# Kernel optimization log

Measured on AMD Instinct MI355X. Metric: run time of the kernel, lower is better.

## Reference

```python
import jax, jax.numpy as jnp
import numpy as np

DIM = 1024
NUM_HEADS = 16
HEAD_DIM = DIM // NUM_HEADS  # 64
H = 32
W = 32
NREG = 8
B = 8
N = H * W + NREG  # 1032


def setup_inputs() -> dict:
    key = jax.random.key(0)
    ks = jax.random.split(key, 6)
    def rn(k, shape, std):
        return jax.random.normal(k, shape, dtype=jnp.float32) * std
    return {
        "x": rn(ks[0], (B, N, DIM), 1.0),
        "qkv_w": rn(ks[1], (3 * DIM, DIM), 0.02),
        "qkv_b": jnp.zeros((3 * DIM,), jnp.float32),
        "proj_w": rn(ks[2], (DIM, DIM), 0.02),
        "proj_b": jnp.zeros((DIM,), jnp.float32),
        "rel_pos_h": rn(ks[3], (2 * H - 1, HEAD_DIM), 0.02),
        "rel_pos_w": rn(ks[4], (2 * W - 1, HEAD_DIM), 0.02),
        "nreg": NREG,
        "cait": 0,
    }


def _rel_pos_table(rel_pos, size):
    # q_size == k_size == size -> relative index = i - j + (size - 1)
    coords = jnp.arange(size)[:, None] - jnp.arange(size)[None, :] + (size - 1)
    return rel_pos[coords]  # (size, size, head_dim)


def reference(x, qkv_w, qkv_b, proj_w, proj_b, rel_pos_h, rel_pos_w, nreg, cait):
    Bx, Nx, C = x.shape
    hd = C // NUM_HEADS
    scale = hd ** (-0.5)
    # qkv: (B, N, 3, nH, hd) -> (3, nH, B, N, hd) -> (3, nH*B, N, hd)
    qkv = (x @ qkv_w.T + qkv_b).reshape(Bx, Nx, 3, NUM_HEADS, hd)
    qkv = jnp.transpose(qkv, (2, 3, 0, 1, 4)).reshape(3, NUM_HEADS * Bx, Nx, hd)
    q, k, v = qkv[0], qkv[1], qkv[2]
    if cait:
        q = q[:, -nreg:]
    attn = jnp.einsum('bqd,bkd->bqk', q * scale, k)  # (nH*B, Nq, N)
    if not cait:
        hw = H * W
        Rh = _rel_pos_table(rel_pos_h, H)  # (H, H, hd)
        Rw = _rel_pos_table(rel_pos_w, W)  # (W, W, hd)
        r_q = q[:, :hw].reshape(-1, H, W, hd)  # unscaled q, grid tokens only
        rel_h = jnp.einsum('bhwc,hkc->bhwk', r_q, Rh)
        rel_w = jnp.einsum('bhwc,wkc->bhwk', r_q, Rw)
        grid = (attn[:, :hw, :hw].reshape(-1, H, W, H, W)
                + rel_h[:, :, :, :, None] + rel_w[:, :, :, None, :])
        attn = attn.at[:, :hw, :hw].set(grid.reshape(-1, hw, hw))
    attn = jax.nn.softmax(attn, axis=-1)
    out = jnp.einsum('bqk,bkd->bqd', attn, v)  # (nH*B, Nq, hd)
    out = out.reshape(NUM_HEADS, Bx, -1, hd)
    out = jnp.transpose(out, (1, 2, 0, 3)).reshape(Bx, -1, C)
    return out @ proj_w.T + proj_b
```

## Files before the change

kernel.cpp:

```cpp
#include <hip/hip_runtime.h>

#define BATCH 8
#define NTOK 1032
#define NPAD 1152
#define MTOT (BATCH*NTOK)
#define MPAD 8320

#define SCALE_Q 0.18033688011112042f
#define C2      5.770780163555854f

typedef __bf16 bf16x8 __attribute__((ext_vector_type(8)));
typedef float f32x4 __attribute__((ext_vector_type(4)));
typedef unsigned short us8 __attribute__((ext_vector_type(8)));
typedef unsigned short us4 __attribute__((ext_vector_type(4)));
typedef short s4 __attribute__((ext_vector_type(4)));

__device__ __forceinline__ unsigned short f2bf(float f){
  unsigned int u = __builtin_bit_cast(unsigned int, f);
  u += 0x7fffu + ((u >> 16) & 1u);
  return (unsigned short)(u >> 16);
}
__device__ __forceinline__ float bf2f(unsigned short u){
  return __builtin_bit_cast(float, (unsigned int)u << 16);
}

#define MFMA16(a,b,c) __builtin_amdgcn_mfma_f32_16x16x32_bf16( \
    __builtin_bit_cast(bf16x8,(a)), __builtin_bit_cast(bf16x8,(b)), (c), 0, 0, 0)
#define MFMAH(a,b,c) __builtin_amdgcn_mfma_f32_16x16x16bf16_1k( \
    __builtin_bit_cast(s4,(a)), __builtin_bit_cast(s4,(b)), (c), 0, 0, 0)

__device__ __forceinline__ void gl_lds16(const unsigned short* g, unsigned short* l){
  __builtin_amdgcn_global_load_lds(
      (const __attribute__((address_space(1))) unsigned int*)g,
      (__attribute__((address_space(3))) unsigned int*)l, 16, 0, 0);
}

__global__ __launch_bounds__(256) void cvt_f32_bf16(const float* __restrict__ in,
                                                    unsigned short* __restrict__ out, int n4){
  int i = blockIdx.x * 256 + threadIdx.x;
  if (i < n4){
    float4 v = reinterpret_cast<const float4*>(in)[i];
    us4 o; o.x = f2bf(v.x); o.y = f2bf(v.y); o.z = f2bf(v.z); o.w = f2bf(v.w);
    reinterpret_cast<us4*>(out)[i] = o;
  }
}

__global__ __launch_bounds__(256) void pad_zero(unsigned short* __restrict__ qb,
                                                unsigned short* __restrict__ kb,
                                                unsigned short* __restrict__ xb,
                                                unsigned short* __restrict__ ao){
  int i = blockIdx.x * 256 + threadIdx.x;
  const int t1 = 128 * (NPAD - NTOK) * 64;
  const int t2 = t1 + (MPAD - MTOT) * 1024;
  const int t3 = t2 + (MPAD - MTOT) * 1024;
  if (i < t1){
    int bh = i / ((NPAD - NTOK) * 64);
    int r  = (i / 64) % (NPAD - NTOK);
    int d  = i % 64;
    int idx = (bh * NPAD + NTOK + r) * 64 + d;
    qb[idx] = 0;
    kb[idx] = 0;
  } else if (i < t2){
    xb[(size_t)MTOT * 1024 + (i - t1)] = 0;
  } else if (i < t3){
    ao[(size_t)MTOT * 1024 + (i - t2)] = 0;
  }
}

__global__ __launch_bounds__(256,4) void qkv_gemm(
    const unsigned short* __restrict__ A,
    const unsigned short* __restrict__ Bw,
    const float* __restrict__ bias,
    unsigned short* __restrict__ qb,
    unsigned short* __restrict__ kb,
    unsigned short* __restrict__ vb)
{
  const int K = 1024;
  __shared__ __align__(16) unsigned short As[2][128*32];
  __shared__ __align__(16) unsigned short Bs[2][128*32];
  int tid = threadIdx.x;
  int id = blockIdx.x;
  int work = (id & 7) * 195 + (id >> 3);
  int m0 = (work / 24) * 128, n0 = (work % 24) * 128;
  int w = tid >> 6, lane = tid & 63, lr = lane & 15, lg = lane >> 4;
  int wr = w >> 1, wc = w & 1;
  int srow = lane >> 2;
  int scol = ((lane & 3) ^ ((lane >> 3) & 3)) * 8;
  int sa = (lg ^ ((lr >> 1) & 3)) * 8;
  f32x4 acc[4][4] = {};

  #pragma unroll
  for (int i = 0; i < 2; i++){
    int q = w * 2 + i;
    gl_lds16(&A [(size_t)(m0 + q*16 + srow) * K + scol], &As[0][q*512]);
    gl_lds16(&Bw[(size_t)(n0 + q*16 + srow) * K + scol], &Bs[0][q*512]);
  }

  for (int kt = 0; kt < 32; kt++){
    int cur = kt & 1;
    if (kt < 31){
      int k0 = (kt + 1) * 32;
      #pragma unroll
      for (int i = 0; i < 2; i++){
        int q = w * 2 + i;
        gl_lds16(&A [(size_t)(m0 + q*16 + srow) * K + k0 + scol], &As[cur^1][q*512]);
        gl_lds16(&Bw[(size_t)(n0 + q*16 + srow) * K + k0 + scol], &Bs[cur^1][q*512]);
      }
      asm volatile("s_waitcnt vmcnt(4)" ::: "memory");
    } else {
      asm volatile("s_waitcnt vmcnt(0)" ::: "memory");
    }
    __builtin_amdgcn_sched_barrier(0);
    __builtin_amdgcn_s_barrier();

    us8 a[4], b[4];
    #pragma unroll
    for (int mi = 0; mi < 4; mi++) a[mi] = *reinterpret_cast<const us8*>(&As[cur][(wr*64 + mi*16 + lr)*32 + sa]);
    #pragma unroll
    for (int ni = 0; ni < 4; ni++) b[ni] = *reinterpret_cast<const us8*>(&Bs[cur][(wc*64 + ni*16 + lr)*32 + sa]);
    #pragma unroll
    for (int mi = 0; mi < 4; mi++)
      #pragma unroll
      for (int ni = 0; ni < 4; ni++)
        acc[mi][ni] = MFMA16(a[mi], b[ni], acc[mi][ni]);
    __builtin_amdgcn_s_barrier();
  }

  #pragma unroll
  for (int mi = 0; mi < 4; mi++){
    #pragma unroll
    for (int ni = 0; ni < 4; ni++){
      #pragma unroll
      for (int reg = 0; reg < 4; reg++){
        int m = m0 + wr*64 + mi*16 + lg*4 + reg;
        if (m >= MTOT) continue;
        int n = n0 + wc*64 + ni*16 + lr;
        float val = acc[mi][ni][reg] + bias[n];
        int b_ = m / NTOK, nidx = m % NTOK;
        int t = n >> 10, h = (n >> 6) & 15, d = n & 63;
        int bh = h * BATCH + b_;
        if (t == 0){
          qb[(size_t)(bh * NPAD + nidx) * 64 + d] = f2bf(val * SCALE_Q);
        } else if (t == 1){
          kb[(size_t)(bh * NPAD + nidx) * 64 + d] = f2bf(val);
        } else {
          vb[(size_t)(bh * NTOK + nidx) * 64 + d] = f2bf(val);
        }
      }
    }
  }
}

__global__ __launch_bounds__(256) void transpose_v(const unsigned short* __restrict__ vb,
                                                   unsigned short* __restrict__ vt){
  __shared__ unsigned short Ls[64][72];
  int blk = blockIdx.x;
  int bh = blk / 17, tl = blk % 17;
  int n0 = tl * 64;
  int t = threadIdx.x;

  #pragma unroll
  for (int p = 0; p < 2; p++){
    int idx = p * 256 + t;
    int r = idx >> 3, c = idx & 7;
    us8 v = {};
    if (n0 + r < NTOK)
      v = *reinterpret_cast<const us8*>(&vb[((size_t)bh * NTOK + n0 + r) * 64 + c * 8]);
    *reinterpret_cast<us8*>(&Ls[r][c * 8]) = v;
  }
  __syncthreads();

  int d = t & 63, ng = t >> 6;
  us8 o[2];
  #pragma unroll
  for (int hf = 0; hf < 2; hf++){
    #pragma unroll
    for (int j = 0; j < 8; j++) o[hf][j] = Ls[ng*16 + hf*8 + j][d];
    *reinterpret_cast<us8*>(&vt[((size_t)bh * 64 + d) * NPAD + n0 + ng*16 + hf*8]) = o[hf];
  }
}

__global__ __launch_bounds__(256,3) void attn_kernel(
    const unsigned short* __restrict__ qb,
    const unsigned short* __restrict__ kb,
    const unsigned short* __restrict__ vt,
    const float* __restrict__ rph,
    const float* __restrict__ rpw,
    unsigned short* __restrict__ ao)
{
  __shared__ __align__(16) unsigned short Ks[2][64*64];
  __shared__ __align__(16) unsigned short Vs[2][64*64];
  __shared__ unsigned short RHt[32*128];
  __shared__ unsigned short RWc[32*128];

  int id = blockIdx.x;
  int work = (id & 7) * 144 + (id >> 3);
  int bh = work / 9;
  int qt = work % 9;
  int tid = threadIdx.x, w = tid >> 6, lane = tid & 63, lr = lane & 15, lg = lane >> 4;
  int h = bh >> 3, b_ = bh & 7;

  const unsigned short* qbase = qb + (size_t)bh * NPAD * 64;
  const unsigned short* kbase = kb + (size_t)bh * NPAD * 64;
  const unsigned short* vbase = vt + (size_t)bh * 64 * NPAD;

  #pragma unroll
  for (int t = 0; t < 2; t++){
    int i = t*256 + tid;
    int row = i >> 3, cs = (i & 7) ^ (row & 7);
    gl_lds16(&kbase[(size_t)row*64 + cs*8],   &Ks[0][(t*256 + w*64)*8]);
    gl_lds16(&vbase[(size_t)row*NPAD + cs*8], &Vs[0][(t*256 + w*64)*8]);
  }

  us8 aq[2][2];
  #pragma unroll
  for (int qf = 0; qf < 2; qf++){
    int qrow = qt*128 + w*32 + qf*16 + lr;
    aq[qf][0] = *reinterpret_cast<const us8*>(&qbase[(size_t)qrow*64 + lg*8]);
    aq[qf][1] = *reinterpret_cast<const us8*>(&qbase[(size_t)qrow*64 + 32 + lg*8]);
  }

  float rwreg[2][2][4] = {};

  if (qt < 8){
    int qh = qt*4 + w;
    f32x4 accH[2][2] = {};
    #pragma unroll
    for (int ks = 0; ks < 2; ks++){
      #pragma unroll
      for (int nf2 = 0; nf2 < 2; nf2++){
        int t = nf2*16 + lr;
        const float* src = rph + (size_t)(qh - t + 31)*64 + ks*32 + lg*8;
        us8 ar;
        #pragma unroll
        for (int j = 0; j < 8; j++) ar[j] = f2bf(src[j]);
        #pragma unroll
        for (int qf = 0; qf < 2; qf++) accH[qf][nf2] = MFMA16(ar, aq[qf][ks], accH[qf][nf2]);
      }
    }
    #pragma unroll
    for (int qf = 0; qf < 2; qf++)
      #pragma unroll
      for (int nf2 = 0; nf2 < 2; nf2++)
        #pragma unroll
        for (int reg = 0; reg < 4; reg++){
          int t_out = nf2*16 + lg*4 + reg;
          RHt[t_out*128 + w*32 + qf*16 + lr] = f2bf(accH[qf][nf2][reg] * 8.0f);
        }
    f32x4 accW[2][4] = {};
    #pragma unroll
    for (int ks = 0; ks < 2; ks++){
      #pragma unroll
      for (int nf = 0; nf < 4; nf++){
        int t = nf*16 + lr;
        us8 aw_ = {};
        if (t < 63){
          const float* src = rpw + (size_t)t*64 + ks*32 + lg*8;
          #pragma unroll
          for (int j = 0; j < 8; j++) aw_[j] = f2bf(src[j]);
        }
        #pragma unroll
        for (int qf = 0; qf < 2; qf++) accW[qf][nf] = MFMA16(aw_, aq[qf][ks], accW[qf][nf]);
      }
    }
    #pragma unroll
    for (int qf = 0; qf < 2; qf++)
      #pragma unroll
      for (int nf = 0; nf < 4; nf++)
        #pragma unroll
        for (int reg = 0; reg < 4; reg++){
          int t_out = nf*16 + lg*4 + reg;
          int qw = qf*16 + lr;
          int kw = qw - t_out + 31;
          if (kw >= 0 && kw < 32)
            RWc[kw*128 + w*32 + qf*16 + lr] = f2bf(accW[qf][nf][reg] * 8.0f);
        }
    #pragma unroll
    for (int qf = 0; qf < 2; qf++)
      #pragma unroll
      for (int hf = 0; hf < 2; hf++)
        #pragma unroll
        for (int reg = 0; reg < 4; reg++)
          rwreg[qf][hf][reg] = bf2f(RWc[(hf*16 + lg*4 + reg)*128 + w*32 + qf*16 + lr]);
  }
  __syncthreads();

  f32x4 O[2][4] = {};
  f32x4 lac[2] = {};
  s4 ones4;
  ones4.x = (short)0x3F80; ones4.y = (short)0x3F80; ones4.z = (short)0x3F80; ones4.w = (short)0x3F80;

  for (int kt = 0; kt < 17; kt++){
    int cur = kt & 1;
    if (kt < 16){
      #pragma unroll
      for (int t = 0; t < 2; t++){
        int i = t*256 + tid;
        int row = i >> 3, cs = (i & 7) ^ (row & 7);
        gl_lds16(&kbase[(size_t)((kt+1)*64 + row)*64 + cs*8], &Ks[cur^1][(t*256 + w*64)*8]);
        gl_lds16(&vbase[(size_t)row*NPAD + (kt+1)*64 + cs*8], &Vs[cur^1][(t*256 + w*64)*8]);
      }
      asm volatile("s_waitcnt vmcnt(4)" ::: "memory");
    } else {
      asm volatile("s_waitcnt vmcnt(0)" ::: "memory");
    }
    __builtin_amdgcn_sched_barrier(0);
    __builtin_amdgcn_s_barrier();

    f32x4 S[2][4] = {};
    __builtin_amdgcn_s_setprio(1);
    #pragma unroll
    for (int ks = 0; ks < 2; ks++)
      #pragma unroll
      for (int nf = 0; nf < 4; nf++){
        us8 bk = *reinterpret_cast<const us8*>(
            &Ks[cur][(nf*16 + lr)*64 + (((ks*4 + lg) ^ (lr & 7)) * 8)]);
        S[0][nf] = MFMA16(bk, aq[0][ks], S[0][nf]);
        S[1][nf] = MFMA16(bk, aq[1][ks], S[1][nf]);
      }
    __builtin_amdgcn_s_setprio(0);

    bool gk = (qt < 8) && (kt < 16);
    float rh2[2][2];
    #pragma unroll
    for (int qf = 0; qf < 2; qf++)
      #pragma unroll
      for (int hf = 0; hf < 2; hf++)
        rh2[qf][hf] = gk ? (bf2f(RHt[(kt*2 + hf)*128 + w*32 + qf*16 + lr]) - C2) : -C2;

    s4 pa[2][4];
    #pragma unroll
    for (int qf = 0; qf < 2; qf++){
      #pragma unroll
      for (int nf = 0; nf < 4; nf++){
        float pv[4];
        #pragma unroll
        for (int reg = 0; reg < 4; reg++){
          float logit = S[qf][nf][reg] + rh2[qf][nf>>1] + (gk ? rwreg[qf][nf&1][reg] : 0.f);
          float p = __builtin_amdgcn_exp2f(logit);
          int key = kt*64 + nf*16 + lg*4 + reg;
          pv[reg] = (key < NTOK) ? p : 0.f;
        }
        unsigned int u0 = __builtin_amdgcn_perm(
            __builtin_bit_cast(unsigned int, pv[1]), __builtin_bit_cast(unsigned int, pv[0]), 0x07060302u);
        unsigned int u1 = __builtin_amdgcn_perm(
            __builtin_bit_cast(unsigned int, pv[3]), __builtin_bit_cast(unsigned int, pv[2]), 0x07060302u);
        uint2 uu; uu.x = u0; uu.y = u1;
        pa[qf][nf] = __builtin_bit_cast(s4, uu);
      }
    }

    __builtin_amdgcn_s_setprio(1);
    #pragma unroll
    for (int qf = 0; qf < 2; qf++)
      #pragma unroll
      for (int nf = 0; nf < 4; nf++)
        lac[qf] = MFMAH(pa[qf][nf], ones4, lac[qf]);
    #pragma unroll
    for (int nf = 0; nf < 4; nf++){
      #pragma unroll
      for (int nfd = 0; nfd < 4; nfd++){
        us4 bv = *reinterpret_cast<const us4*>(
            &Vs[cur][(nfd*16 + lr)*64 + (((nf*2 + (lg>>1)) ^ (lr & 7))*8) + (lg&1)*4]);
        O[0][nfd] = MFMAH(pa[0][nf], bv, O[0][nfd]);
        O[1][nfd] = MFMAH(pa[1][nf], bv, O[1][nfd]);
      }
    }
    __builtin_amdgcn_s_setprio(0);
    __builtin_amdgcn_s_barrier();
  }

  #pragma unroll
  for (int qf = 0; qf < 2; qf++)
    #pragma unroll
    for (int reg = 0; reg < 4; reg++){
      int qg = qt*128 + w*32 + qf*16 + lg*4 + reg;
      if (qg < NTOK){
        float inv = 1.0f / lac[qf][reg];
        #pragma unroll
        for (int nfd = 0; nfd < 4; nfd++)
          ao[(size_t)(b_ * NTOK + qg) * 1024 + h*64 + nfd*16 + lr] = f2bf(O[qf][nfd][reg] * inv);
      }
    }
}

__global__ __launch_bounds__(256,4) void proj_gemm(
    const unsigned short* __restrict__ A,
    const unsigned short* __restrict__ Bw,
    const float* __restrict__ bias,
    float* __restrict__ out)
{
  const int K = 1024;
  __shared__ __align__(16) unsigned short As[2][128*32];
  __shared__ __align__(16) unsigned short Bs[2][128*32];
  int tid = threadIdx.x;
  int id = blockIdx.x;
  int work = (id & 7) * 65 + (id >> 3);
  int m0 = (work / 8) * 128, n0 = (work % 8) * 128;
  int w = tid >> 6, lane = tid & 63, lr = lane & 15, lg = lane >> 4;
  int wr = w >> 1, wc = w & 1;
  int srow = lane >> 2;
  int scol = ((lane & 3) ^ ((lane >> 3) & 3)) * 8;
  int sa = (lg ^ ((lr >> 1) & 3)) * 8;
  f32x4 acc[4][4] = {};

  #pragma unroll
  for (int i = 0; i < 2; i++){
    int q = w * 2 + i;
    gl_lds16(&A [(size_t)(m0 + q*16 + srow) * K + scol], &As[0][q*512]);
    gl_lds16(&Bw[(size_t)(n0 + q*16 + srow) * K + scol], &Bs[0][q*512]);
  }

  for (int kt = 0; kt < 32; kt++){
    int cur = kt & 1;
    if (kt < 31){
      int k0 = (kt + 1) * 32;
      #pragma unroll
      for (int i = 0; i < 2; i++){
        int q = w * 2 + i;
        gl_lds16(&A [(size_t)(m0 + q*16 + srow) * K + k0 + scol], &As[cur^1][q*512]);
        gl_lds16(&Bw[(size_t)(n0 + q*16 + srow) * K + k0 + scol], &Bs[cur^1][q*512]);
      }
      asm volatile("s_waitcnt vmcnt(4)" ::: "memory");
    } else {
      asm volatile("s_waitcnt vmcnt(0)" ::: "memory");
    }
    __builtin_amdgcn_sched_barrier(0);
    __builtin_amdgcn_s_barrier();

    us8 a[4], b[4];
    #pragma unroll
    for (int mi = 0; mi < 4; mi++) a[mi] = *reinterpret_cast<const us8*>(&As[cur][(wr*64 + mi*16 + lr)*32 + sa]);
    #pragma unroll
    for (int ni = 0; ni < 4; ni++) b[ni] = *reinterpret_cast<const us8*>(&Bs[cur][(wc*64 + ni*16 + lr)*32 + sa]);
    #pragma unroll
    for (int mi = 0; mi < 4; mi++)
      #pragma unroll
      for (int ni = 0; ni < 4; ni++)
        acc[mi][ni] = MFMA16(a[mi], b[ni], acc[mi][ni]);
    __builtin_amdgcn_s_barrier();
  }

  #pragma unroll
  for (int mi = 0; mi < 4; mi++){
    #pragma unroll
    for (int ni = 0; ni < 4; ni++){
      #pragma unroll
      for (int reg = 0; reg < 4; reg++){
        int m = m0 + wr*64 + mi*16 + lg*4 + reg;
        if (m >= MTOT) continue;
        int n = n0 + wc*64 + ni*16 + lr;
        out[(size_t)m * 1024 + n] = acc[mi][ni][reg] + bias[n];
      }
    }
  }
}

extern "C" void kernel_launch(void* const* d_in, const int* in_sizes, int n_in,
                              void* d_out, int out_size, void* d_ws, size_t ws_size,
                              hipStream_t stream)
{
  const float* x      = (const float*)d_in[0];
  const float* qkv_w  = (const float*)d_in[1];
  const float* qkv_b  = (const float*)d_in[2];
  const float* proj_w = (const float*)d_in[3];
  const float* proj_b = (const float*)d_in[4];
  const float* rph    = (const float*)d_in[5];
  const float* rpw    = (const float*)d_in[6];
  float* out = (float*)d_out;

  char* ws = (char*)d_ws;
  size_t off = 0;
  auto alloc = [&](size_t bytes){ char* p = ws + off; off += (bytes + 255) & ~(size_t)255; return p; };
  unsigned short* x_bf  = (unsigned short*)alloc((size_t)MPAD * 1024 * 2);
  unsigned short* qw_bf = (unsigned short*)alloc((size_t)3072 * 1024 * 2);
  unsigned short* pw_bf = (unsigned short*)alloc((size_t)1024 * 1024 * 2);
  unsigned short* qbuf  = (unsigned short*)alloc((size_t)128 * NPAD * 64 * 2);
  unsigned short* kbuf  = (unsigned short*)alloc((size_t)128 * NPAD * 64 * 2);
  unsigned short* vtbuf = (unsigned short*)alloc((size_t)128 * 64 * NPAD * 2);
  unsigned short* aout  = (unsigned short*)alloc((size_t)MPAD * 1024 * 2);
  if (off > ws_size) return;

  unsigned short* vbuf = aout;

  int n4x = MTOT * 1024 / 4;
  cvt_f32_bf16<<<dim3((n4x + 255) / 256), 256, 0, stream>>>(x, x_bf, n4x);
  int n4q = 3072 * 1024 / 4;
  cvt_f32_bf16<<<dim3((n4q + 255) / 256), 256, 0, stream>>>(qkv_w, qw_bf, n4q);
  int n4p = 1024 * 1024 / 4;
  cvt_f32_bf16<<<dim3((n4p + 255) / 256), 256, 0, stream>>>(proj_w, pw_bf, n4p);

  int npad = 128 * (NPAD - NTOK) * 64 + 2 * (MPAD - MTOT) * 1024;
  pad_zero<<<dim3((npad + 255) / 256), 256, 0, stream>>>(qbuf, kbuf, x_bf, aout);

  qkv_gemm<<<dim3(1560), 256, 0, stream>>>(x_bf, qw_bf, qkv_b, qbuf, kbuf, vbuf);
  transpose_v<<<dim3(128 * 17), 256, 0, stream>>>(vbuf, vtbuf);
  attn_kernel<<<dim3(1152), 256, 0, stream>>>(qbuf, kbuf, vtbuf, rph, rpw, aout);
  proj_gemm<<<dim3(520), 256, 0, stream>>>(aout, pw_bf, proj_b, out);
}
```

Baseline: 226.0 us.

## Enlarge QKV and projection GEMM tiles to 256x256 with 512-thread blocks

Both GEMMs move from 128x128 tiles with K-step 32 and 4 waves to 256x256 tiles with K-step 64, 8 waves per 512-thread block, and a new XOR LDS swizzle. Prefetch loads for the next K tile are spread across four sub-phases of MFMA work, with s_setprio raised around the MFMAs, and the XCD-aware tile mapping is recomputed for the new grid sizes. The larger tiles raise arithmetic intensity and cut global traffic, and MPAD grows to cover 256-row tiles. In exchange, LDS use per block is higher and occupancy drops to one block per CU, and the grid now has far fewer blocks.

```diff
diff --git a/kernel.cpp b/kernel.cpp
--- a/kernel.cpp
+++ b/kernel.cpp
@@ -4,7 +4,7 @@
 #define NTOK 1032
 #define NPAD 1152
 #define MTOT (BATCH*NTOK)
-#define MPAD 8320
+#define MPAD 8448
 
 #define SCALE_Q 0.18033688011112042f
 #define C2      5.770780163555854f
@@ -67,7 +67,7 @@
   }
 }
 
-__global__ __launch_bounds__(256,4) void qkv_gemm(
+__global__ __launch_bounds__(512,1) void qkv_gemm(
     const unsigned short* __restrict__ A,
     const unsigned short* __restrict__ Bw,
     const float* __restrict__ bias,
@@ -75,73 +75,108 @@
     unsigned short* __restrict__ kb,
     unsigned short* __restrict__ vb)
 {
-  const int K = 1024;
-  __shared__ __align__(16) unsigned short As[2][128*32];
-  __shared__ __align__(16) unsigned short Bs[2][128*32];
+  const int K = 1024, NT = 16;
+  __shared__ __align__(16) unsigned short LA[2][2][128*64];
+  __shared__ __align__(16) unsigned short LB[2][2][128*64];
   int tid = threadIdx.x;
-  int id = blockIdx.x;
-  int work = (id & 7) * 195 + (id >> 3);
-  int m0 = (work / 24) * 128, n0 = (work % 24) * 128;
   int w = tid >> 6, lane = tid & 63, lr = lane & 15, lg = lane >> 4;
-  int wr = w >> 1, wc = w & 1;
-  int srow = lane >> 2;
-  int scol = ((lane & 3) ^ ((lane >> 3) & 3)) * 8;
-  int sa = (lg ^ ((lr >> 1) & 3)) * 8;
-  f32x4 acc[4][4] = {};
-
-  #pragma unroll
-  for (int i = 0; i < 2; i++){
-    int q = w * 2 + i;
-    gl_lds16(&A [(size_t)(m0 + q*16 + srow) * K + scol], &As[0][q*512]);
-    gl_lds16(&Bw[(size_t)(n0 + q*16 + srow) * K + scol], &Bs[0][q*512]);
-  }
-
-  for (int kt = 0; kt < 32; kt++){
-    int cur = kt & 1;
-    if (kt < 31){
-      int k0 = (kt + 1) * 32;
-      #pragma unroll
-      for (int i = 0; i < 2; i++){
-        int q = w * 2 + i;
-        gl_lds16(&A [(size_t)(m0 + q*16 + srow) * K + k0 + scol], &As[cur^1][q*512]);
-        gl_lds16(&Bw[(size_t)(n0 + q*16 + srow) * K + k0 + scol], &Bs[cur^1][q*512]);
-      }
-      asm volatile("s_waitcnt vmcnt(4)" ::: "memory");
-    } else {
-      asm volatile("s_waitcnt vmcnt(0)" ::: "memory");
-    }
-    __builtin_amdgcn_sched_barrier(0);
-    __builtin_amdgcn_s_barrier();
-
-    us8 a[4], b[4];
-    #pragma unroll
-    for (int mi = 0; mi < 4; mi++) a[mi] = *reinterpret_cast<const us8*>(&As[cur][(wr*64 + mi*16 + lr)*32 + sa]);
-    #pragma unroll
-    for (int ni = 0; ni < 4; ni++) b[ni] = *reinterpret_cast<const us8*>(&Bs[cur][(wc*64 + ni*16 + lr)*32 + sa]);
-    #pragma unroll
-    for (int mi = 0; mi < 4; mi++)
-      #pragma unroll
-      for (int ni = 0; ni < 4; ni++)
-        acc[mi][ni] = MFMA16(a[mi], b[ni], acc[mi][ni]);
-    __builtin_amdgcn_s_barrier();
-  }
-
-  #pragma unroll
-  for (int mi = 0; mi < 4; mi++){
-    #pragma unroll
-    for (int ni = 0; ni < 4; ni++){
+  int wr = w >> 2, wc = w & 3;
+
+  int orig = blockIdx.x, xcd = orig & 7;
+  int wgid = (xcd < 4 ? xcd * 50 : 200 + (xcd - 4) * 49) + (orig >> 3);
+  int m0 = (wgid / 12) * 256, n0 = (wgid % 12) * 256;
+
+  int srow = lane >> 3;
+  int scol = ((lane & 7) ^ (srow & 7)) * 8;
+  int c2 = w * 2;
+  int rsw = lr & 7;
+
+  auto stA = [&](int buf, int h, int k0){
+    #pragma unroll
+    for (int i = 0; i < 2; i++)
+      gl_lds16(&A[(size_t)(m0 + h*128 + (c2+i)*8 + srow) * K + k0 + scol],
+               &LA[buf][h][(c2+i)*512]);
+  };
+  auto stB = [&](int buf, int h, int k0){
+    #pragma unroll
+    for (int i = 0; i < 2; i++)
+      gl_lds16(&Bw[(size_t)(n0 + h*128 + (c2+i)*8 + srow) * K + k0 + scol],
+               &LB[buf][h][(c2+i)*512]);
+  };
+
+  f32x4 acc[8][4] = {};
+
+  stA(0,0,0); stA(0,1,0); stB(0,0,0); stB(0,1,0);
+  asm volatile("s_waitcnt vmcnt(0)" ::: "memory");
+  __builtin_amdgcn_s_barrier();
+
+  for (int t = 0; t < NT; t++){
+    int buf = t & 1, nbuf = buf ^ 1, k0n = (t+1) * 64;
+    bool pre = (t+1 < NT);
+    const unsigned short* Abase = &LA[buf][wr][0];
+    const unsigned short* Bbase = &LB[buf][wc>>1][0];
+    us8 bfr[4][2];
+    #pragma unroll
+    for (int p = 0; p < 4; p++){
+      if (p == 0){
+        #pragma unroll
+        for (int nf = 0; nf < 4; nf++)
+          #pragma unroll
+          for (int kk = 0; kk < 2; kk++){
+            int brow = (wc & 1)*64 + nf*16 + lr;
+            int slot = (kk*4 + lg) ^ rsw;
+            bfr[nf][kk] = *reinterpret_cast<const us8*>(&Bbase[brow*64 + slot*8]);
+          }
+      }
+      us8 afr[2][2];
+      #pragma unroll
+      for (int j = 0; j < 2; j++)
+        #pragma unroll
+        for (int kk = 0; kk < 2; kk++){
+          int arow = p*32 + j*16 + lr;
+          int slot = (kk*4 + lg) ^ rsw;
+          afr[j][kk] = *reinterpret_cast<const us8*>(&Abase[arow*64 + slot*8]);
+        }
+      if (pre){
+        if (p == 0){ stA(nbuf, 0, k0n); stA(nbuf, 1, k0n); }
+        else if (p == 1){ stB(nbuf, 0, k0n); }
+        else if (p == 2){ stB(nbuf, 1, k0n); }
+      }
+      __builtin_amdgcn_sched_barrier(0);
+      __builtin_amdgcn_s_barrier();
+      __builtin_amdgcn_s_setprio(1);
+      #pragma unroll
+      for (int kk = 0; kk < 2; kk++)
+        #pragma unroll
+        for (int j = 0; j < 2; j++)
+          #pragma unroll
+          for (int nf = 0; nf < 4; nf++)
+            acc[2*p+j][nf] = MFMA16(afr[j][kk], bfr[nf][kk], acc[2*p+j][nf]);
+      __builtin_amdgcn_s_setprio(0);
+      if (p == 3)
+        asm volatile("s_waitcnt vmcnt(0)" ::: "memory");
+      __builtin_amdgcn_sched_barrier(0);
+      __builtin_amdgcn_s_barrier();
+    }
+  }
+
+  #pragma unroll
+  for (int nf = 0; nf < 4; nf++){
+    int n = n0 + wc*64 + nf*16 + lr;
+    float bs = bias[n];
+    int tsel = n >> 10, h = (n >> 6) & 15, d = n & 63;
+    #pragma unroll
+    for (int fm = 0; fm < 8; fm++){
       #pragma unroll
       for (int reg = 0; reg < 4; reg++){
-        int m = m0 + wr*64 + mi*16 + lg*4 + reg;
+        int m = m0 + wr*128 + fm*16 + lg*4 + reg;
         if (m >= MTOT) continue;
-        int n = n0 + wc*64 + ni*16 + lr;
-        float val = acc[mi][ni][reg] + bias[n];
+        float val = acc[fm][nf][reg] + bs;
         int b_ = m / NTOK, nidx = m % NTOK;
-        int t = n >> 10, h = (n >> 6) & 15, d = n & 63;
         int bh = h * BATCH + b_;
-        if (t == 0){
+        if (tsel == 0){
           qb[(size_t)(bh * NPAD + nidx) * 64 + d] = f2bf(val * SCALE_Q);
-        } else if (t == 1){
+        } else if (tsel == 1){
           kb[(size_t)(bh * NPAD + nidx) * 64 + d] = f2bf(val);
         } else {
           vb[(size_t)(bh * NTOK + nidx) * 64 + d] = f2bf(val);
@@ -384,73 +419,108 @@
     }
 }
 
-__global__ __launch_bounds__(256,4) void proj_gemm(
+__global__ __launch_bounds__(512,1) void proj_gemm(
     const unsigned short* __restrict__ A,
     const unsigned short* __restrict__ Bw,
     const float* __restrict__ bias,
     float* __restrict__ out)
 {
-  const int K = 1024;
-  __shared__ __align__(16) unsigned short As[2][128*32];
-  __shared__ __align__(16) unsigned short Bs[2][128*32];
+  const int K = 1024, NT = 16;
+  __shared__ __align__(16) unsigned short LA[2][2][128*64];
+  __shared__ __align__(16) unsigned short LB[2][2][128*64];
   int tid = threadIdx.x;
-  int id = blockIdx.x;
-  int work = (id & 7) * 65 + (id >> 3);
-  int m0 = (work / 8) * 128, n0 = (work % 8) * 128;
   int w = tid >> 6, lane = tid & 63, lr = lane & 15, lg = lane >> 4;
-  int wr = w >> 1, wc = w & 1;
-  int srow = lane >> 2;
-  int scol = ((lane & 3) ^ ((lane >> 3) & 3)) * 8;
-  int sa = (lg ^ ((lr >> 1) & 3)) * 8;
-  f32x4 acc[4][4] = {};
-
-  #pragma unroll
-  for (int i = 0; i < 2; i++){
-    int q = w * 2 + i;
-    gl_lds16(&A [(size_t)(m0 + q*16 + srow) * K + scol], &As[0][q*512]);
-    gl_lds16(&Bw[(size_t)(n0 + q*16 + srow) * K + scol], &Bs[0][q*512]);
-  }
-
-  for (int kt = 0; kt < 32; kt++){
-    int cur = kt & 1;
-    if (kt < 31){
-      int k0 = (kt + 1) * 32;
-      #pragma unroll
-      for (int i = 0; i < 2; i++){
-        int q = w * 2 + i;
-        gl_lds16(&A [(size_t)(m0 + q*16 + srow) * K + k0 + scol], &As[cur^1][q*512]);
-        gl_lds16(&Bw[(size_t)(n0 + q*16 + srow) * K + k0 + scol], &Bs[cur^1][q*512]);
-      }
-      asm volatile("s_waitcnt vmcnt(4)" ::: "memory");
-    } else {
-      asm volatile("s_waitcnt vmcnt(0)" ::: "memory");
-    }
-    __builtin_amdgcn_sched_barrier(0);
-    __builtin_amdgcn_s_barrier();
-
-    us8 a[4], b[4];
-    #pragma unroll
-    for (int mi = 0; mi < 4; mi++) a[mi] = *reinterpret_cast<const us8*>(&As[cur][(wr*64 + mi*16 + lr)*32 + sa]);
-    #pragma unroll
-    for (int ni = 0; ni < 4; ni++) b[ni] = *reinterpret_cast<const us8*>(&Bs[cur][(wc*64 + ni*16 + lr)*32 + sa]);
-    #pragma unroll
-    for (int mi = 0; mi < 4; mi++)
-      #pragma unroll
-      for (int ni = 0; ni < 4; ni++)
-        acc[mi][ni] = MFMA16(a[mi], b[ni], acc[mi][ni]);
-    __builtin_amdgcn_s_barrier();
-  }
-
-  #pragma unroll
-  for (int mi = 0; mi < 4; mi++){
-    #pragma unroll
-    for (int ni = 0; ni < 4; ni++){
+  int wr = w >> 2, wc = w & 3;
+
+  int orig = blockIdx.x, xcd = orig & 7;
+  int wgid = (xcd < 4 ? xcd * 17 : 68 + (xcd - 4) * 16) + (orig >> 3);
+  int m0 = (wgid / 4) * 256, n0 = (wgid % 4) * 256;
+
+  int srow = lane >> 3;
+  int scol = ((lane & 7) ^ (srow & 7)) * 8;
+  int c2 = w * 2;
+  int rsw = lr & 7;
+
+  auto stA = [&](int buf, int h, int k0){
+    #pragma unroll
+    for (int i = 0; i < 2; i++)
+      gl_lds16(&A[(size_t)(m0 + h*128 + (c2+i)*8 + srow) * K + k0 + scol],
+               &LA[buf][h][(c2+i)*512]);
+  };
+  auto stB = [&](int buf, int h, int k0){
+    #pragma unroll
+    for (int i = 0; i < 2; i++)
+      gl_lds16(&Bw[(size_t)(n0 + h*128 + (c2+i)*8 + srow) * K + k0 + scol],
+               &LB[buf][h][(c2+i)*512]);
+  };
+
+  f32x4 acc[8][4] = {};
+
+  stA(0,0,0); stA(0,1,0); stB(0,0,0); stB(0,1,0);
+  asm volatile("s_waitcnt vmcnt(0)" ::: "memory");
+  __builtin_amdgcn_s_barrier();
+
+  for (int t = 0; t < NT; t++){
+    int buf = t & 1, nbuf = buf ^ 1, k0n = (t+1) * 64;
+    bool pre = (t+1 < NT);
+    const unsigned short* Abase = &LA[buf][wr][0];
+    const unsigned short* Bbase = &LB[buf][wc>>1][0];
+    us8 bfr[4][2];
+    #pragma unroll
+    for (int p = 0; p < 4; p++){
+      if (p == 0){
+        #pragma unroll
+        for (int nf = 0; nf < 4; nf++)
+          #pragma unroll
+          for (int kk = 0; kk < 2; kk++){
+            int brow = (wc & 1)*64 + nf*16 + lr;
+            int slot = (kk*4 + lg) ^ rsw;
+            bfr[nf][kk] = *reinterpret_cast<const us8*>(&Bbase[brow*64 + slot*8]);
+          }
+      }
+      us8 afr[2][2];
+      #pragma unroll
+      for (int j = 0; j < 2; j++)
+        #pragma unroll
+        for (int kk = 0; kk < 2; kk++){
+          int arow = p*32 + j*16 + lr;
+          int slot = (kk*4 + lg) ^ rsw;
+          afr[j][kk] = *reinterpret_cast<const us8*>(&Abase[arow*64 + slot*8]);
+        }
+      if (pre){
+        if (p == 0){ stA(nbuf, 0, k0n); stA(nbuf, 1, k0n); }
+        else if (p == 1){ stB(nbuf, 0, k0n); }
+        else if (p == 2){ stB(nbuf, 1, k0n); }
+      }
+      __builtin_amdgcn_sched_barrier(0);
+      __builtin_amdgcn_s_barrier();
+      __builtin_amdgcn_s_setprio(1);
+      #pragma unroll
+      for (int kk = 0; kk < 2; kk++)
+        #pragma unroll
+        for (int j = 0; j < 2; j++)
+          #pragma unroll
+          for (int nf = 0; nf < 4; nf++)
+            acc[2*p+j][nf] = MFMA16(afr[j][kk], bfr[nf][kk], acc[2*p+j][nf]);
+      __builtin_amdgcn_s_setprio(0);
+      if (p == 3)
+        asm volatile("s_waitcnt vmcnt(0)" ::: "memory");
+      __builtin_amdgcn_sched_barrier(0);
+      __builtin_amdgcn_s_barrier();
+    }
+  }
+
+  #pragma unroll
+  for (int nf = 0; nf < 4; nf++){
+    int n = n0 + wc*64 + nf*16 + lr;
+    float bs = bias[n];
+    #pragma unroll
+    for (int fm = 0; fm < 8; fm++){
       #pragma unroll
       for (int reg = 0; reg < 4; reg++){
-        int m = m0 + wr*64 + mi*16 + lg*4 + reg;
+        int m = m0 + wr*128 + fm*16 + lg*4 + reg;
         if (m >= MTOT) continue;
-        int n = n0 + wc*64 + ni*16 + lr;
-        out[(size_t)m * 1024 + n] = acc[mi][ni][reg] + bias[n];
+        out[(size_t)m * 1024 + n] = acc[fm][nf][reg] + bs;
       }
     }
   }
@@ -493,8 +563,8 @@
   int npad = 128 * (NPAD - NTOK) * 64 + 2 * (MPAD - MTOT) * 1024;
   pad_zero<<<dim3((npad + 255) / 256), 256, 0, stream>>>(qbuf, kbuf, x_bf, aout);
 
-  qkv_gemm<<<dim3(1560), 256, 0, stream>>>(x_bf, qw_bf, qkv_b, qbuf, kbuf, vbuf);
+  qkv_gemm<<<dim3(396), 512, 0, stream>>>(x_bf, qw_bf, qkv_b, qbuf, kbuf, vbuf);
   transpose_v<<<dim3(128 * 17), 256, 0, stream>>>(vbuf, vtbuf);
   attn_kernel<<<dim3(1152), 256, 0, stream>>>(qbuf, kbuf, vtbuf, rph, rpw, aout);
-  proj_gemm<<<dim3(520), 256, 0, stream>>>(aout, pw_bf, proj_b, out);
-}
+  proj_gemm<<<dim3(132), 512, 0, stream>>>(aout, pw_bf, proj_b, out);
+}
```

Result: slower. 259.3 us (+14.7%).
